# Optimization experiments

Hardware: AMD Instinct MI355X
Metric: run time of the kernel (lower is better)

Reference implementation:

```python
import jax, jax.numpy as jnp
import numpy as np

NUM_HEADS = 8
HEAD_DIM = 64
HIDDEN_SIZE = 128
TOP_K = 16
EPS = 1e-6


def setup_inputs() -> dict:
    key = jax.random.key(0)
    k1, k2, k3 = jax.random.split(key, 3)
    B, H, S, D = 4, NUM_HEADS, 1024, HEAD_DIM
    return {
        "keys": jax.random.normal(k1, (B, H, S, D), dtype=jnp.float32),
        "values": jax.random.normal(k2, (B, H, S, D), dtype=jnp.float32),
        "queries": jax.random.normal(k3, (B, H, S, D), dtype=jnp.float32),
    }


def _project(x):
    # replicate [B,H,S,D] along last dim to cover HIDDEN_SIZE basis indices
    D = x.shape[-1]
    if D >= HIDDEN_SIZE:
        return x[..., :HIDDEN_SIZE]
    repeats = (HIDDEN_SIZE + D - 1) // D
    return jnp.tile(x, (1, 1, 1, repeats))[..., :HIDDEN_SIZE]


def reference(keys, values, queries):
    B, H, S, D = keys.shape
    b_idx = jnp.arange(B)[:, None, None]   # [B,1,1]
    h_idx = jnp.arange(H)[None, :, None]   # [1,H,1]

    # ---- update: scatter-add outer products into assigned memory bank ----
    assignments = jnp.argmax(jnp.abs(_project(keys)), axis=-1)  # [B,H,S]
    outer = values[..., :, None] * keys[..., None, :]           # [B,H,S,D,D] (v k^T)
    M = jnp.zeros((B, H, HIDDEN_SIZE, D, D), dtype=keys.dtype)
    M = M.at[b_idx, h_idx, assignments].add(outer)
    z = jnp.zeros((B, H, HIDDEN_SIZE, D), dtype=keys.dtype)
    z = z.at[b_idx, h_idx, assignments].add(keys)

    # ---- retrieve: top-k basis selection, gather-matvec, weighted combine ----
    scores = jnp.abs(_project(queries))                          # [B,H,S,HIDDEN]
    top_scores, top_idx = jax.lax.top_k(scores, TOP_K)           # [B,H,S,K]
    weights = jax.nn.softmax(top_scores, axis=-1)

    output = jnp.zeros((B, H, S, D), dtype=queries.dtype)
    for k in range(TOP_K):
        mem = top_idx[..., k]                                    # [B,H,S]
        M_sel = M[b_idx, h_idx, mem]                             # [B,H,S,D,D]
        z_sel = z[b_idx, h_idx, mem]                             # [B,H,S,D]
        num = jnp.einsum('bhsde,bhse->bhsd', M_sel, queries)
        den = jnp.einsum('bhsd,bhsd->bhs', z_sel, queries)[..., None] + EPS
        output = output + weights[..., k:k + 1] * (num / den)
    return output
```

## Files before the change

kernel.cpp:

```cpp
#include <hip/hip_runtime.h>
#include <math.h>

#define S_LEN 1024
#define EPS 1e-6f

typedef __attribute__((ext_vector_type(8)))  short bf16x8;
typedef __attribute__((ext_vector_type(4)))  short bf16x4;
typedef __attribute__((ext_vector_type(16))) float float16v;


__device__ __forceinline__ void wave_argmax(float& bv, int& bi) {
    #pragma unroll
    for (int off = 1; off < 64; off <<= 1) {
        float ov = __shfl_xor(bv, off, 64);
        int   oi = __shfl_xor(bi, off, 64);
        if (ov > bv || (ov == bv && oi < bi)) { bv = ov; bi = oi; }
    }
}

__device__ __forceinline__ unsigned short f2bf(float f) {
    unsigned int u = __float_as_uint(f);
    unsigned int r = (u + 0x7fffu + ((u >> 16) & 1u)) >> 16;
    return (unsigned short)r;
}

__device__ __forceinline__ bf16x8 pack8(float4 a, float4 b) {
    bf16x8 r;
    r[0] = (short)f2bf(a.x); r[1] = (short)f2bf(a.y);
    r[2] = (short)f2bf(a.z); r[3] = (short)f2bf(a.w);
    r[4] = (short)f2bf(b.x); r[5] = (short)f2bf(b.y);
    r[6] = (short)f2bf(b.z); r[7] = (short)f2bf(b.w);
    return r;
}

__global__ __launch_bounds__(256) void k_pre(const float* __restrict__ keys,
                                             const float* __restrict__ queries,
                                             int* __restrict__ kcnt2,
                                             unsigned short* __restrict__ klist2,
                                             int* __restrict__ qcnt2,
                                             unsigned* __restrict__ qpair,
                                             float* __restrict__ out) {
    const int bh   = blockIdx.x >> 5;
    const int blk  = blockIdx.x & 31;
    const int wv   = threadIdx.x >> 6;
    const int lane = threadIdx.x & 63;

    __shared__ int khist[64], qhist[64];
    if (threadIdx.x < 64) { khist[threadIdx.x] = 0; qhist[threadIdx.x] = 0; }
    __syncthreads();

    const int s0 = blk * 32 + wv * 8;
    float kv[8], qv[8];
    #pragma unroll
    for (int i = 0; i < 8; ++i) {
        kv[i] = keys   [((size_t)bh * 1024 + s0 + i) * 64 + lane];
        qv[i] = queries[((size_t)bh * 1024 + s0 + i) * 64 + lane];
    }

    {
        float4 zz = {0.f, 0.f, 0.f, 0.f};
        float4* po = (float4*)(out + (size_t)blockIdx.x * 2048);
        po[threadIdx.x] = zz; po[threadIdx.x + 256] = zz;
    }

    #pragma unroll
    for (int i = 0; i < 8; ++i) {
        float bv = fabsf(kv[i]); int bi = lane;
        wave_argmax(bv, bi);
        if (lane == 0) {
            int pos = atomicAdd(&khist[bi], 1);
            klist2[((size_t)bh * 64 + bi) * 1024 + blk * 32 + pos] =
                (unsigned short)(s0 + i);
        }
    }

    #pragma unroll
    for (int i = 0; i < 8; ++i) {
        unsigned ud = __float_as_uint(qv[i]) & 0x7fffffffu;
        int gt = 0;
        #pragma unroll
        for (int k = 0; k < 64; ++k) {
            unsigned ui = (unsigned)__builtin_amdgcn_readlane((int)ud, k);
            gt += (ui > ud) ? 1 : 0;
        }
        int S = gt;
        #pragma unroll
        for (int off = 1; off < 64; off <<= 1) S += __shfl_xor(S, off, 64);
        float e = expf(__uint_as_float(ud));
        int copies, contrib;
        if (S == 2016) {
            contrib = (gt < 8);
            copies  = contrib ? 2 : 0;
        } else {
            int eq = 0, eql = 0;
            #pragma unroll
            for (int k = 0; k < 64; ++k) {
                unsigned ui = (unsigned)__builtin_amdgcn_readlane((int)ud, k);
                eq  += (ui == ud) ? 1 : 0;
                eql += (ui == ud && k < lane) ? 1 : 0;
            }
            int pos_low  = 2 * gt + eql;
            int pos_high = pos_low + eq;
            copies  = (pos_low < 16 ? 1 : 0) + (pos_high < 16 ? 1 : 0);
            contrib = (pos_low < 16);
        }
        float ce = (float)copies * e;
        #pragma unroll
        for (int off = 1; off < 64; off <<= 1) ce += __shfl_xor(ce, off, 64);
        if (contrib) {
            int pos = atomicAdd(&qhist[lane], 1);
            unsigned wb = __float_as_uint(e / ce) & 0xFFFFFC00u;
            qpair[((size_t)bh * 64 + lane) * 1024 + blk * 32 + pos] =
                wb | (unsigned)(s0 + i);
        }
    }
    __syncthreads();
    if (threadIdx.x < 64) {
        kcnt2[(bh * 32 + blk) * 64 + threadIdx.x] = khist[threadIdx.x];
        qcnt2[(bh * 32 + blk) * 64 + threadIdx.x] = qhist[threadIdx.x];
    }
}

__global__ __launch_bounds__(256) void k_main(const float* __restrict__ keys,
                                              const float* __restrict__ values,
                                              const float* __restrict__ queries,
                                              const int* __restrict__ kcnt2,
                                              const unsigned short* __restrict__ klist2,
                                              const int* __restrict__ qcnt2,
                                              const unsigned* __restrict__ qpair,
                                              float* __restrict__ out) {
    const int g     = blockIdx.x;
    const int bh    = g >> 6;
    const int bank  = g & 63;
    const int t     = threadIdx.x;
    const int lane  = t & 63;
    const int grp   = t >> 6;

    __shared__ alignas(16) unsigned short M_bf[64 * 64];
    __shared__ alignas(16) unsigned short Q_bf[64 * 64];
    __shared__ alignas(16) unsigned short Ou_bf[64 * 68];
    __shared__ unsigned short s_match[256];
    __shared__ unsigned q_ent[256];
    __shared__ int    koffs_s[33], qoffs_s[33];
    __shared__ float  z_s[64];
    __shared__ double den_s[64];
    __shared__ float  w_s[2][64];
    __shared__ int    sq_s[2][64];

    if (t < 64) {
        int i = t & 31;
        int c = (t < 32) ? kcnt2[(bh * 32 + i) * 64 + bank]
                         : qcnt2[(bh * 32 + i) * 64 + bank];
        #pragma unroll
        for (int off = 1; off < 32; off <<= 1) {
            int o = __shfl(c, t - off, 64);
            if (i >= off) c += o;
        }
        if (t < 32) { if (i == 0) koffs_s[0] = 0; koffs_s[i + 1] = c; }
        else        { if (i == 0) qoffs_s[0] = 0; qoffs_s[i + 1] = c; }
    }
    __syncthreads();

    const int nm = koffs_s[32];
    const int nq = qoffs_s[32];
    if (nm == 0 || nq == 0) return;

    float acc[16];
    #pragma unroll
    for (int m = 0; m < 16; ++m) acc[m] = 0.f;
    float zacc = 0.f;
    const float* kb = keys   + (size_t)bh * S_LEN * 64;
    const float* vb = values + (size_t)bh * S_LEN * 64;
    int it = 0;
    for (int cb = 0; cb < nm; cb += 256) {
        const int cn = min(256, nm - cb);
        __syncthreads();
        if (t < cn) {
            int idx = cb + t;
            int seg = 0;
            #pragma unroll
            for (int i = 1; i < 32; ++i) if (idx >= koffs_s[i]) seg = i;
            s_match[t] = klist2[(size_t)(bh * 64 + bank) * 1024 + seg * 32 +
                                (idx - koffs_s[seg])];
        }
        __syncthreads();
        for (int base = 0; base < cn; base += 8, ++it) {
            float* kst = (float*)Ou_bf + (it & 1) * 1024;
            float* vst = kst + 512;
            #pragma unroll
            for (int rr = 0; rr < 2; ++rr) {
                int row = grp + rr * 4;
                if (base + row < cn) {
                    int s = s_match[base + row];
                    kst[row * 64 + lane] = kb[(size_t)s * 64 + lane];
                    vst[row * 64 + lane] = vb[(size_t)s * 64 + lane];
                }
            }
            __syncthreads();
            int lim = min(8, cn - base);
            for (int jj = 0; jj < lim; ++jj) {
                float kv = kst[jj * 64 + lane];
                #pragma unroll
                for (int m = 0; m < 16; ++m)
                    acc[m] += vst[jj * 64 + grp * 16 + m] * kv;
            }
            if (t < 64)
                for (int jj = 0; jj < lim; ++jj) zacc += kst[jj * 64 + t];
        }
    }
    #pragma unroll
    for (int m = 0; m < 16; ++m) {
        int dv = grp * 16 + m;
        M_bf[dv * 64 + (((lane >> 3) ^ (dv & 7)) << 3) + (lane & 7)] = f2bf(acc[m]);
    }
    if (t < 64) z_s[t] = zacc;

    const float* qb = queries + (size_t)bh * S_LEN * 64;
    float*       ob = out     + (size_t)bh * S_LEN * 64;
    const int dvh = grp >> 1, jh = grp & 1;
    const int hi  = lane >> 5;

    int prev_nb = 0;
    for (int qbase = 0, batch = 0; qbase < nq; qbase += 64, ++batch) {
        const int nb  = min(64, nq - qbase);
        const int cur = batch & 1;

        if ((qbase & 255) == 0) {
            if (qbase + t < nq) {
                int jg = qbase + t;
                int seg = 0;
                #pragma unroll
                for (int i = 1; i < 32; ++i) if (jg >= qoffs_s[i]) seg = i;
                q_ent[t] = qpair[(size_t)(bh * 64 + bank) * 1024 + seg * 32 +
                                 (jg - qoffs_s[seg])];
            }
            __syncthreads();
        }

        if (batch > 0) {
            #pragma unroll
            for (int jj = 0; jj < 16; ++jj) {
                int j = grp * 16 + jj;
                if (j < prev_nb) {
                    float v = __uint_as_float((unsigned)Ou_bf[j * 68 + lane] << 16);
                    unsafeAtomicAdd(&ob[(size_t)sq_s[1 - cur][j] * 64 + lane], v);
                }
            }
        }
        {
            int j = t >> 2, c4 = t & 3;
            bf16x8 p0 = {}, p1 = {};
            double d = 0.0;
            if (j < nb) {
                unsigned e = q_ent[(qbase & 255) + j];
                int s = (int)(e & 1023u);
                if ((t & 3) == 0) {
                    sq_s[cur][j] = s;
                    w_s[cur][j]  = __uint_as_float(e & 0xFFFFFC00u);
                }
                const float4* src = (const float4*)(qb + (size_t)s * 64 + c4 * 16);
                float4 f0 = src[0], f1 = src[1], f2 = src[2], f3 = src[3];
                p0 = pack8(f0, f1);
                p1 = pack8(f2, f3);
                const float4* zz4 = (const float4*)&z_s[c4 * 16];
                float4 z0 = zz4[0], z1 = zz4[1], z2 = zz4[2], z3 = zz4[3];
                d  = (double)z0.x * f0.x + (double)z0.y * f0.y + (double)z0.z * f0.z + (double)z0.w * f0.w;
                d += (double)z1.x * f1.x + (double)z1.y * f1.y + (double)z1.z * f1.z + (double)z1.w * f1.w;
                d += (double)z2.x * f2.x + (double)z2.y * f2.y + (double)z2.z * f2.z + (double)z2.w * f2.w;
                d += (double)z3.x * f3.x + (double)z3.y * f3.y + (double)z3.z * f3.z + (double)z3.w * f3.w;
            }
            int c0 = c4 * 2;
            *(bf16x8*)&Q_bf[j * 64 + ((c0 ^ (j & 7)) << 3)]       = p0;
            *(bf16x8*)&Q_bf[j * 64 + (((c0 + 1) ^ (j & 7)) << 3)] = p1;
            d += __shfl_xor(d, 1, 64);
            d += __shfl_xor(d, 2, 64);
            if ((t & 3) == 0) den_s[j] = d;
        }
        __syncthreads();

        float16v C;
        #pragma unroll
        for (int i = 0; i < 16; ++i) C[i] = 0.f;
        const int am = dvh * 32 + (lane & 31);
        const int bn = jh  * 32 + (lane & 31);
        #pragma unroll
        for (int ks = 0; ks < 4; ++ks) {
            int ch = ks * 2 + hi;
            bf16x8 af = *(const bf16x8*)&M_bf[am * 64 + ((ch ^ (am & 7)) << 3)];
            bf16x8 bf = *(const bf16x8*)&Q_bf[bn * 64 + ((ch ^ (bn & 7)) << 3)];
            C = __builtin_amdgcn_mfma_f32_32x32x16_bf16(af, bf, C, 0, 0, 0);
        }
        {
            double den = den_s[bn];
            float  w   = w_s[cur][bn];
            float rinv = (float)((double)w / (den + (double)EPS));
            #pragma unroll
            for (int rq = 0; rq < 4; ++rq) {
                bf16x4 pk;
                pk[0] = (short)f2bf(C[rq * 4 + 0] * rinv);
                pk[1] = (short)f2bf(C[rq * 4 + 1] * rinv);
                pk[2] = (short)f2bf(C[rq * 4 + 2] * rinv);
                pk[3] = (short)f2bf(C[rq * 4 + 3] * rinv);
                *(bf16x4*)&Ou_bf[bn * 68 + dvh * 32 + rq * 8 + hi * 4] = pk;
            }
        }
        __syncthreads();
        prev_nb = nb;
    }
    {
        const int cur = (((nq + 63) >> 6) - 1) & 1;
        #pragma unroll
        for (int jj = 0; jj < 16; ++jj) {
            int j = grp * 16 + jj;
            if (j < prev_nb) {
                float v = __uint_as_float((unsigned)Ou_bf[j * 68 + lane] << 16);
                unsafeAtomicAdd(&ob[(size_t)sq_s[cur][j] * 64 + lane], v);
            }
        }
    }
}

extern "C" void kernel_launch(void* const* d_in, const int* in_sizes, int n_in,
                              void* d_out, int out_size, void* d_ws, size_t ws_size,
                              hipStream_t stream) {
    const float* keys    = (const float*)d_in[0];
    const float* values  = (const float*)d_in[1];
    const float* queries = (const float*)d_in[2];
    char* ws = (char*)d_ws;
    int*            kcnt2  = (int*)(ws);
    int*            qcnt2  = (int*)(ws + 262144);
    unsigned short* klist2 = (unsigned short*)(ws + 524288);
    unsigned*       qpair  = (unsigned*)(ws + 4718592);

    k_pre <<<1024, 256, 0, stream>>>(keys, queries, kcnt2, klist2, qcnt2, qpair,
                                     (float*)d_out);
    k_main<<<2048, 256, 0, stream>>>(keys, values, queries, kcnt2, klist2, qcnt2, qpair,
                                     (float*)d_out);
}
```

Before: 161.4 us.

## Split memory build into separate kernel and halve query work per block

Memory-bank construction (M and z accumulation) moves into a new k_build kernel that writes bf16 M and z to workspace. The main kernel now launches two blocks per (bh, bank), each handling half of the matched queries and loading the prebuilt M from global memory. This raises parallelism and evens out per-block load, at the cost of an extra launch and a global round trip for M. When the workspace is too small, it falls back to rebuilding M in each split block, which duplicates that work.

```diff
diff --git a/kernel.cpp b/kernel.cpp
--- a/kernel.cpp
+++ b/kernel.cpp
@@ -121,49 +121,38 @@
     }
 }
 
-__global__ __launch_bounds__(256) void k_main(const float* __restrict__ keys,
-                                              const float* __restrict__ values,
-                                              const float* __restrict__ queries,
-                                              const int* __restrict__ kcnt2,
-                                              const unsigned short* __restrict__ klist2,
-                                              const int* __restrict__ qcnt2,
-                                              const unsigned* __restrict__ qpair,
-                                              float* __restrict__ out) {
-    const int g     = blockIdx.x;
-    const int bh    = g >> 6;
-    const int bank  = g & 63;
-    const int t     = threadIdx.x;
-    const int lane  = t & 63;
-    const int grp   = t >> 6;
-
-    __shared__ alignas(16) unsigned short M_bf[64 * 64];
-    __shared__ alignas(16) unsigned short Q_bf[64 * 64];
-    __shared__ alignas(16) unsigned short Ou_bf[64 * 68];
+__global__ __launch_bounds__(256) void k_build(const float* __restrict__ keys,
+                                               const float* __restrict__ values,
+                                               const int* __restrict__ kcnt2,
+                                               const unsigned short* __restrict__ klist2,
+                                               unsigned short* __restrict__ M_g,
+                                               float* __restrict__ z_g,
+                                               int* __restrict__ nm_g) {
+    const int g    = blockIdx.x;
+    const int bh   = g >> 6;
+    const int bank = g & 63;
+    const int t    = threadIdx.x;
+    const int lane = t & 63;
+    const int grp  = t >> 6;
+
+    __shared__ float stg[2][1024];
     __shared__ unsigned short s_match[256];
-    __shared__ unsigned q_ent[256];
-    __shared__ int    koffs_s[33], qoffs_s[33];
-    __shared__ float  z_s[64];
-    __shared__ double den_s[64];
-    __shared__ float  w_s[2][64];
-    __shared__ int    sq_s[2][64];
-
-    if (t < 64) {
-        int i = t & 31;
-        int c = (t < 32) ? kcnt2[(bh * 32 + i) * 64 + bank]
-                         : qcnt2[(bh * 32 + i) * 64 + bank];
+    __shared__ int koffs_s[33];
+
+    if (t < 32) {
+        int c = kcnt2[(bh * 32 + t) * 64 + bank];
         #pragma unroll
         for (int off = 1; off < 32; off <<= 1) {
             int o = __shfl(c, t - off, 64);
-            if (i >= off) c += o;
-        }
-        if (t < 32) { if (i == 0) koffs_s[0] = 0; koffs_s[i + 1] = c; }
-        else        { if (i == 0) qoffs_s[0] = 0; qoffs_s[i + 1] = c; }
+            if (t >= off) c += o;
+        }
+        if (t == 0) koffs_s[0] = 0;
+        koffs_s[t + 1] = c;
     }
     __syncthreads();
-
     const int nm = koffs_s[32];
-    const int nq = qoffs_s[32];
-    if (nm == 0 || nq == 0) return;
+    if (t == 0) nm_g[g] = nm;
+    if (nm == 0) return;
 
     float acc[16];
     #pragma unroll
@@ -185,7 +174,7 @@
         }
         __syncthreads();
         for (int base = 0; base < cn; base += 8, ++it) {
-            float* kst = (float*)Ou_bf + (it & 1) * 1024;
+            float* kst = stg[it & 1];
             float* vst = kst + 512;
             #pragma unroll
             for (int rr = 0; rr < 2; ++rr) {
@@ -208,26 +197,153 @@
                 for (int jj = 0; jj < lim; ++jj) zacc += kst[jj * 64 + t];
         }
     }
+    unsigned short* mg = M_g + (size_t)g * 4096;
     #pragma unroll
     for (int m = 0; m < 16; ++m) {
         int dv = grp * 16 + m;
-        M_bf[dv * 64 + (((lane >> 3) ^ (dv & 7)) << 3) + (lane & 7)] = f2bf(acc[m]);
-    }
-    if (t < 64) z_s[t] = zacc;
+        mg[dv * 64 + (((lane >> 3) ^ (dv & 7)) << 3) + (lane & 7)] = f2bf(acc[m]);
+    }
+    if (t < 64) z_g[(size_t)g * 64 + t] = zacc;
+}
+
+template <bool GM>
+__global__ __launch_bounds__(256) void k_main_t(const float* __restrict__ keys,
+                                                const float* __restrict__ values,
+                                                const float* __restrict__ queries,
+                                                const int* __restrict__ kcnt2,
+                                                const unsigned short* __restrict__ klist2,
+                                                const int* __restrict__ qcnt2,
+                                                const unsigned* __restrict__ qpair,
+                                                const unsigned short* __restrict__ M_g,
+                                                const float* __restrict__ z_g,
+                                                const int* __restrict__ nm_g,
+                                                float* __restrict__ out) {
+    const int g     = blockIdx.x;
+    const int gb    = g >> 1;
+    const int split = g & 1;
+    const int bh    = gb >> 6;
+    const int bank  = gb & 63;
+    const int t     = threadIdx.x;
+    const int lane  = t & 63;
+    const int grp   = t >> 6;
+
+    __shared__ alignas(16) unsigned short M_bf[64 * 64];
+    __shared__ alignas(16) unsigned short Q_bf[64 * 64];
+    __shared__ alignas(16) unsigned short Ou_bf[64 * 68];
+    __shared__ unsigned short s_match[256];
+    __shared__ unsigned q_ent[256];
+    __shared__ int    koffs_s[33], qoffs_s[33];
+    __shared__ float  z_s[64];
+    __shared__ double den_s[64];
+    __shared__ float  w_s[2][64];
+    __shared__ int    sq_s[2][64];
+
+    if constexpr (GM) {
+        if (t < 32) {
+            int c = qcnt2[(bh * 32 + t) * 64 + bank];
+            #pragma unroll
+            for (int off = 1; off < 32; off <<= 1) {
+                int o = __shfl(c, t - off, 64);
+                if (t >= off) c += o;
+            }
+            if (t == 0) qoffs_s[0] = 0;
+            qoffs_s[t + 1] = c;
+        }
+    } else {
+        if (t < 64) {
+            int i = t & 31;
+            int c = (t < 32) ? kcnt2[(bh * 32 + i) * 64 + bank]
+                             : qcnt2[(bh * 32 + i) * 64 + bank];
+            #pragma unroll
+            for (int off = 1; off < 32; off <<= 1) {
+                int o = __shfl(c, t - off, 64);
+                if (i >= off) c += o;
+            }
+            if (t < 32) { if (i == 0) koffs_s[0] = 0; koffs_s[i + 1] = c; }
+            else        { if (i == 0) qoffs_s[0] = 0; qoffs_s[i + 1] = c; }
+        }
+    }
+    __syncthreads();
+
+    const int nq   = qoffs_s[32];
+    const int half = (nq + 1) >> 1;
+    const int jlo  = split * half;
+    const int jhi  = min(nq, jlo + half);
+    int nm;
+    if constexpr (GM) nm = nm_g[gb]; else nm = koffs_s[32];
+    if (nm == 0 || jhi <= jlo) return;
+
+    if constexpr (GM) {
+        const unsigned short* mg = M_g + (size_t)gb * 4096;
+        *(bf16x8*)&M_bf[t * 8]        = *(const bf16x8*)&mg[t * 8];
+        *(bf16x8*)&M_bf[2048 + t * 8] = *(const bf16x8*)&mg[2048 + t * 8];
+        if (t < 64) z_s[t] = z_g[(size_t)gb * 64 + t];
+    } else {
+        float acc[16];
+        #pragma unroll
+        for (int m = 0; m < 16; ++m) acc[m] = 0.f;
+        float zacc = 0.f;
+        const float* kb = keys   + (size_t)bh * S_LEN * 64;
+        const float* vb = values + (size_t)bh * S_LEN * 64;
+        int it = 0;
+        for (int cb = 0; cb < nm; cb += 256) {
+            const int cn = min(256, nm - cb);
+            __syncthreads();
+            if (t < cn) {
+                int idx = cb + t;
+                int seg = 0;
+                #pragma unroll
+                for (int i = 1; i < 32; ++i) if (idx >= koffs_s[i]) seg = i;
+                s_match[t] = klist2[(size_t)(bh * 64 + bank) * 1024 + seg * 32 +
+                                    (idx - koffs_s[seg])];
+            }
+            __syncthreads();
+            for (int base = 0; base < cn; base += 8, ++it) {
+                float* kst = (float*)Ou_bf + (it & 1) * 1024;
+                float* vst = kst + 512;
+                #pragma unroll
+                for (int rr = 0; rr < 2; ++rr) {
+                    int row = grp + rr * 4;
+                    if (base + row < cn) {
+                        int s = s_match[base + row];
+                        kst[row * 64 + lane] = kb[(size_t)s * 64 + lane];
+                        vst[row * 64 + lane] = vb[(size_t)s * 64 + lane];
+                    }
+                }
+                __syncthreads();
+                int lim = min(8, cn - base);
+                for (int jj = 0; jj < lim; ++jj) {
+                    float kv = kst[jj * 64 + lane];
+                    #pragma unroll
+                    for (int m = 0; m < 16; ++m)
+                        acc[m] += vst[jj * 64 + grp * 16 + m] * kv;
+                }
+                if (t < 64)
+                    for (int jj = 0; jj < lim; ++jj) zacc += kst[jj * 64 + t];
+            }
+        }
+        #pragma unroll
+        for (int m = 0; m < 16; ++m) {
+            int dv = grp * 16 + m;
+            M_bf[dv * 64 + (((lane >> 3) ^ (dv & 7)) << 3) + (lane & 7)] = f2bf(acc[m]);
+        }
+        if (t < 64) z_s[t] = zacc;
+    }
 
     const float* qb = queries + (size_t)bh * S_LEN * 64;
     float*       ob = out     + (size_t)bh * S_LEN * 64;
     const int dvh = grp >> 1, jh = grp & 1;
     const int hi  = lane >> 5;
+    const int nqL = jhi - jlo;
 
     int prev_nb = 0;
-    for (int qbase = 0, batch = 0; qbase < nq; qbase += 64, ++batch) {
-        const int nb  = min(64, nq - qbase);
+    for (int qloc = 0, batch = 0; qloc < nqL; qloc += 64, ++batch) {
+        const int nb  = min(64, nqL - qloc);
         const int cur = batch & 1;
 
-        if ((qbase & 255) == 0) {
-            if (qbase + t < nq) {
-                int jg = qbase + t;
+        if ((qloc & 255) == 0) {
+            if (qloc + t < nqL) {
+                int jg = jlo + qloc + t;
                 int seg = 0;
                 #pragma unroll
                 for (int i = 1; i < 32; ++i) if (jg >= qoffs_s[i]) seg = i;
@@ -252,7 +368,7 @@
             bf16x8 p0 = {}, p1 = {};
             double d = 0.0;
             if (j < nb) {
-                unsigned e = q_ent[(qbase & 255) + j];
+                unsigned e = q_ent[(qloc & 255) + j];
                 int s = (int)(e & 1023u);
                 if ((t & 3) == 0) {
                     sq_s[cur][j] = s;
@@ -308,7 +424,7 @@
         prev_nb = nb;
     }
     {
-        const int cur = (((nq + 63) >> 6) - 1) & 1;
+        const int cur = (((nqL + 63) >> 6) - 1) & 1;
         #pragma unroll
         for (int jj = 0; jj < 16; ++jj) {
             int j = grp * 16 + jj;
@@ -331,9 +447,22 @@
     int*            qcnt2  = (int*)(ws + 262144);
     unsigned short* klist2 = (unsigned short*)(ws + 524288);
     unsigned*       qpair  = (unsigned*)(ws + 4718592);
-
-    k_pre <<<1024, 256, 0, stream>>>(keys, queries, kcnt2, klist2, qcnt2, qpair,
-                                     (float*)d_out);
-    k_main<<<2048, 256, 0, stream>>>(keys, values, queries, kcnt2, klist2, qcnt2, qpair,
-                                     (float*)d_out);
-}
+    unsigned short* M_g    = (unsigned short*)(ws + 13107200);
+    float*          z_g    = (float*)(ws + 29884416);
+    int*            nm_g   = (int*)(ws + 30408704);
+    const bool big = (ws_size >= 30416896u);
+
+    k_pre<<<1024, 256, 0, stream>>>(keys, queries, kcnt2, klist2, qcnt2, qpair,
+                                    (float*)d_out);
+    if (big) {
+        k_build<<<2048, 256, 0, stream>>>(keys, values, kcnt2, klist2,
+                                          M_g, z_g, nm_g);
+        k_main_t<true><<<4096, 256, 0, stream>>>(keys, values, queries, kcnt2,
+                                                 klist2, qcnt2, qpair,
+                                                 M_g, z_g, nm_g, (float*)d_out);
+    } else {
+        k_main_t<false><<<4096, 256, 0, stream>>>(keys, values, queries, kcnt2,
+                                                  klist2, qcnt2, qpair,
+                                                  M_g, z_g, nm_g, (float*)d_out);
+    }
+}
```

Measured after the change: 168.7 us. 4.5% more time.
